# Optimization experiments

Hardware: AMD Instinct MI355X
Metric: run time of the kernel (lower is better)

Reference implementation:

```python
import jax, jax.numpy as jnp
import numpy as np

B, T, C = 4, 2048, 2048
H, G = 16, 4            # num_heads, gqa_factor
HKV = H // G            # kv heads = 4
D = C // H              # head_dim = 128
KV = HKV * D            # kv_embed_dim = 512


def setup_inputs() -> dict:
    key = jax.random.key(0)
    ks = jax.random.split(key, 6)
    w_scale = (2.0 / (C + C)) ** 0.5  # xavier-uniform-ish std
    return {
        "query": jax.random.normal(ks[0], (B, T, C), jnp.float32),
        "key": jax.random.normal(ks[1], (B, T, C), jnp.float32),
        "value": jax.random.normal(ks[2], (B, T, C), jnp.float32),
        "in_proj_weight": jax.random.normal(ks[3], (C + 2 * KV, C), jnp.float32) * w_scale,
        "in_proj_bias": jnp.zeros((C + 2 * KV,), jnp.float32),
        "out_proj_weight": jax.random.normal(ks[4], (C, C), jnp.float32) * w_scale,
        "out_proj_bias": jnp.zeros((C,), jnp.float32),
    }


def reference(query, key, value, in_proj_weight, in_proj_bias, out_proj_weight, out_proj_bias):
    # split fused QKV projection (rows: [C | KV | KV])
    qw, kw, vw = in_proj_weight[:C], in_proj_weight[C:C + KV], in_proj_weight[C + KV:]
    qb, kb, vb = in_proj_bias[:C], in_proj_bias[C:C + KV], in_proj_bias[C + KV:]

    xq = query @ qw.T + qb          # (B,T,C)
    xk = key @ kw.T + kb            # (B,T,KV)
    xv = value @ vw.T + vb          # (B,T,KV)

    # (B,T,G,Hkv,D) -> (B,G,Hkv,T,D)
    xq = xq.reshape(B, T, G, HKV, D).transpose(0, 2, 3, 1, 4)
    # (B,T,Hkv,D) -> (B,Hkv,T,D); broadcast over G in attention
    xk = xk.reshape(B, T, HKV, D).transpose(0, 2, 1, 3)
    xv = xv.reshape(B, T, HKV, D).transpose(0, 2, 1, 3)

    scale = 1.0 / jnp.sqrt(jnp.asarray(D, xq.dtype))
    scores = jnp.einsum("bghtd,bhsd->bghts", xq, xk) * scale  # (B,G,Hkv,T,T)
    causal = jnp.tril(jnp.ones((T, T), bool))
    scores = jnp.where(causal, scores, jnp.finfo(scores.dtype).min)
    attn = jax.nn.softmax(scores, axis=-1)

    xo = jnp.einsum("bghts,bhsd->bghtd", attn, xv)            # (B,G,Hkv,T,D)
    xo = xo.transpose(0, 3, 1, 2, 4).reshape(B, T, C)          # (B,T,C)
    return xo @ out_proj_weight.T + out_proj_bias
```

## Files before the change

### kernel.cpp

```cpp
#include <hip/hip_runtime.h>
#include <hip/hip_bf16.h>
#include <stdint.h>

#define B_ 4
#define T_ 2048
#define C_ 2048
#define H_ 16
#define HKV_ 4
#define D_ 128
#define KV_ 512

typedef __attribute__((ext_vector_type(8))) short bf16x8;
typedef __attribute__((ext_vector_type(4))) float f32x4;

__device__ __forceinline__ unsigned short f2bf(float f) {
    union { float f; unsigned int u; } c;
    c.f = f;
    unsigned int u = c.u;
    u += 0x7FFFu + ((u >> 16) & 1u);
    return (unsigned short)(u >> 16);
}

__global__ __launch_bounds__(256)
void f32_to_bf16(const float* __restrict__ src, unsigned short* __restrict__ dst, int n4)
{
    int i = blockIdx.x * 256 + threadIdx.x;
    if (i < n4) {
        float4 v = ((const float4*)src)[i];
        ushort4 o;
        o.x = f2bf(v.x); o.y = f2bf(v.y); o.z = f2bf(v.z); o.w = f2bf(v.w);
        ((ushort4*)dst)[i] = o;
    }
}

template <typename OutT, bool TRANS>
__global__ __launch_bounds__(256)
void gemm_bt_bias(const __hip_bfloat16* __restrict__ A,
                  const __hip_bfloat16* __restrict__ W,
                  const float* __restrict__ bias,
                  OutT* __restrict__ Cmat,
                  int M, int N, int K)
{
    __shared__ __align__(16) __hip_bfloat16 lA[128 * 32];
    __shared__ __align__(16) __hip_bfloat16 lB[128 * 32];

    const int tid  = threadIdx.x;
    const int wave = tid >> 6;
    const int lane = tid & 63;
    const int m0 = blockIdx.x * 128;
    const int n0 = blockIdx.y * 128;
    const int wm = (wave >> 1) * 64;
    const int wn = (wave & 1) * 64;
    const int srow = lane >> 2;
    const int scol = (lane & 3) * 8;
    const int quad = lane >> 4;
    const int r16  = lane & 15;

    f32x4 acc[4][4];
#pragma unroll
    for (int i = 0; i < 4; ++i)
#pragma unroll
        for (int j = 0; j < 4; ++j)
            acc[i][j] = (f32x4){0.f, 0.f, 0.f, 0.f};

    const __hip_bfloat16* gA = A + (size_t)(m0 + wave * 16 + srow) * K + scol;
    const __hip_bfloat16* gB = W + (size_t)(n0 + wave * 16 + srow) * K + scol;

    for (int k0 = 0; k0 < K; k0 += 32) {
        __builtin_amdgcn_global_load_lds(
            (const __attribute__((address_space(1))) void*)(gA + k0),
            (__attribute__((address_space(3))) void*)(lA + wave * 16 * 32), 16, 0, 0);
        __builtin_amdgcn_global_load_lds(
            (const __attribute__((address_space(1))) void*)(gA + (size_t)64 * K + k0),
            (__attribute__((address_space(3))) void*)(lA + (64 + wave * 16) * 32), 16, 0, 0);
        __builtin_amdgcn_global_load_lds(
            (const __attribute__((address_space(1))) void*)(gB + k0),
            (__attribute__((address_space(3))) void*)(lB + wave * 16 * 32), 16, 0, 0);
        __builtin_amdgcn_global_load_lds(
            (const __attribute__((address_space(1))) void*)(gB + (size_t)64 * K + k0),
            (__attribute__((address_space(3))) void*)(lB + (64 + wave * 16) * 32), 16, 0, 0);
        __syncthreads();

        bf16x8 af[4], bfr[4];
#pragma unroll
        for (int i = 0; i < 4; ++i)
            af[i] = *(const bf16x8*)(lA + (wm + i * 16 + r16) * 32 + quad * 8);
#pragma unroll
        for (int j = 0; j < 4; ++j)
            bfr[j] = *(const bf16x8*)(lB + (wn + j * 16 + r16) * 32 + quad * 8);
#pragma unroll
        for (int i = 0; i < 4; ++i)
#pragma unroll
            for (int j = 0; j < 4; ++j)
                acc[i][j] = __builtin_amdgcn_mfma_f32_16x16x32_bf16(
                    af[i], bfr[j], acc[i][j], 0, 0, 0);
        __syncthreads();
    }

#pragma unroll
    for (int i = 0; i < 4; ++i) {
        const int row = m0 + wm + i * 16 + quad * 4;
#pragma unroll
        for (int j = 0; j < 4; ++j) {
            const int col = n0 + wn + j * 16 + r16;
            const float bb = bias[col];
            if constexpr (TRANS) {
                const int bb_idx = row >> 11;
                const int t = row & (T_ - 1);
                ushort4 o;
                o.x = f2bf(acc[i][j][0] + bb);
                o.y = f2bf(acc[i][j][1] + bb);
                o.z = f2bf(acc[i][j][2] + bb);
                o.w = f2bf(acc[i][j][3] + bb);
                *(ushort4*)((unsigned short*)Cmat +
                            ((size_t)(bb_idx * N + col)) * T_ + t) = o;
            } else {
#pragma unroll
                for (int r = 0; r < 4; ++r) {
                    const float v = acc[i][j][r] + bb;
                    if constexpr (sizeof(OutT) == 4) {
                        Cmat[(size_t)(row + r) * N + col] = v;
                    } else {
                        ((unsigned short*)Cmat)[(size_t)(row + r) * N + col] = f2bf(v);
                    }
                }
            }
        }
    }
}

__global__ __launch_bounds__(512)
void attn_flash(const __hip_bfloat16* __restrict__ xq,
                const __hip_bfloat16* __restrict__ xk,
                const __hip_bfloat16* __restrict__ xvT,
                __hip_bfloat16* __restrict__ xo)
{
    __shared__ __align__(16) __hip_bfloat16 lK[2][64 * 128];
    __shared__ __align__(16) __hip_bfloat16 lV[2][128 * 64];
    __shared__ __align__(16) __hip_bfloat16 lP[8 * 32 * 64];

    const int tid  = threadIdx.x;
    const int wave = tid >> 6;
    const int lane = tid & 63;
    const int quad = lane >> 4;
    const int r16  = lane & 15;
    const int sw8  = (r16 & 7) * 8;
    const int q0 = blockIdx.x * 256;
    const int h  = blockIdx.y;
    const int b  = blockIdx.z;
    const int hkv = h & (HKV_ - 1);
    const int r0 = q0 + wave * 32;
    const float SC2 = 0.12751879215f;
    const float SH2 = 17.3123404907f;

    bf16x8 qf[2][4];
#pragma unroll
    for (int i = 0; i < 2; ++i)
#pragma unroll
        for (int kc = 0; kc < 4; ++kc)
            qf[i][kc] = *(const bf16x8*)(
                xq + ((size_t)(b * T_ + r0 + i * 16 + r16)) * C_ +
                h * D_ + kc * 32 + quad * 8);

    f32x4 oacc[2][8];
#pragma unroll
    for (int i = 0; i < 2; ++i)
#pragma unroll
        for (int db = 0; db < 8; ++db)
            oacc[i][db] = (f32x4){0.f, 0.f, 0.f, 0.f};
    float lrow[2][4];
#pragma unroll
    for (int i = 0; i < 2; ++i)
#pragma unroll
        for (int r = 0; r < 4; ++r) lrow[i][r] = 0.f;

    const __hip_bfloat16* kb = xk + ((size_t)b * T_) * KV_ + hkv * D_;
    const __hip_bfloat16* vb = xvT + ((size_t)(b * KV_ + hkv * D_)) * T_;
    __hip_bfloat16* lPw = lP + wave * 32 * 64;

    const int krl  = lane >> 4;
    const int ksw  = ((lane & 15) ^ (((wave & 1) * 4) + krl)) * 8;
    const int vrl  = lane >> 3;
    const int vsw  = ((lane & 7) ^ vrl) * 8;

    const int ntiles = q0 / 64 + 4;

    auto STAGE = [&](int buf, int tile) {
        const int s0 = tile * 64;
        __hip_bfloat16* lKb = &lK[buf][0];
        __hip_bfloat16* lVb = &lV[buf][0];
#pragma unroll
        for (int q = 0; q < 2; ++q) {
            __builtin_amdgcn_global_load_lds(
                (const __attribute__((address_space(1))) void*)(
                    kb + (size_t)(s0 + q * 32 + wave * 4 + krl) * KV_ + ksw),
                (__attribute__((address_space(3))) void*)(lKb + (q * 32 + wave * 4) * 128),
                16, 0, 0);
            __builtin_amdgcn_global_load_lds(
                (const __attribute__((address_space(1))) void*)(
                    vb + (size_t)(q * 64 + wave * 8 + vrl) * T_ + s0 + vsw),
                (__attribute__((address_space(3))) void*)(lVb + (q * 64 + wave * 8) * 64),
                16, 0, 0);
        }
    };

    STAGE(0, 0);
    __syncthreads();

    for (int tile = 0; tile < ntiles; ++tile) {
        const int cur = tile & 1;
        const int s0 = tile * 64;

        if (tile + 1 < ntiles) STAGE(cur ^ 1, tile + 1);

        const __hip_bfloat16* lKc = &lK[cur][0];
        const __hip_bfloat16* lVc = &lV[cur][0];

        if (s0 <= r0 + 31) {
            const bool diag = (s0 + 63 > r0);

            f32x4 sacc[2][4];
#pragma unroll
            for (int i = 0; i < 2; ++i)
#pragma unroll
                for (int j = 0; j < 4; ++j)
                    sacc[i][j] = (f32x4){0.f, 0.f, 0.f, 0.f};
#pragma unroll
            for (int kc = 0; kc < 4; ++kc) {
                bf16x8 kf[4];
#pragma unroll
                for (int j = 0; j < 4; ++j)
                    kf[j] = *(const bf16x8*)(lKc + (j * 16 + r16) * 128 +
                                             ((kc * 32 + quad * 8) ^ sw8));
#pragma unroll
                for (int i = 0; i < 2; ++i)
#pragma unroll
                    for (int j = 0; j < 4; ++j)
                        sacc[i][j] = __builtin_amdgcn_mfma_f32_16x16x32_bf16(
                            qf[i][kc], kf[j], sacc[i][j], 0, 0, 0);
            }

#pragma unroll
            for (int i = 0; i < 2; ++i) {
#pragma unroll
                for (int j = 0; j < 4; ++j)
#pragma unroll
                    for (int r = 0; r < 4; ++r) {
                        float p = exp2f(fmaf(sacc[i][j][r], SC2, -SH2));
                        if (diag) {
                            const int rr = r0 + i * 16 + quad * 4 + r;
                            const int cc = s0 + j * 16 + r16;
                            if (cc > rr) p = 0.f;
                        }
                        lrow[i][r] += p;
                        const int prow = i * 16 + quad * 4 + r;
                        ((unsigned short*)lPw)[prow * 64 +
                            ((j * 16 + r16) ^ (((quad * 4 + r) & 7) * 8))] = f2bf(p);
                    }
            }

#pragma unroll
            for (int sc = 0; sc < 2; ++sc) {
                bf16x8 pf[2];
#pragma unroll
                for (int i = 0; i < 2; ++i)
                    pf[i] = *(const bf16x8*)(lPw + (i * 16 + r16) * 64 +
                                             ((sc * 32 + quad * 8) ^ sw8));
#pragma unroll
                for (int db = 0; db < 8; ++db) {
                    const bf16x8 vf = *(const bf16x8*)(lVc + (db * 16 + r16) * 64 +
                                                       ((sc * 32 + quad * 8) ^ sw8));
#pragma unroll
                    for (int i = 0; i < 2; ++i)
                        oacc[i][db] = __builtin_amdgcn_mfma_f32_16x16x32_bf16(
                            pf[i], vf, oacc[i][db], 0, 0, 0);
                }
            }
        }
        __syncthreads();
    }

#pragma unroll
    for (int i = 0; i < 2; ++i) {
#pragma unroll
        for (int off = 1; off <= 8; off <<= 1)
#pragma unroll
            for (int r = 0; r < 4; ++r)
                lrow[i][r] += __shfl_xor(lrow[i][r], off);
        float inv[4];
#pragma unroll
        for (int r = 0; r < 4; ++r) inv[r] = 1.0f / lrow[i][r];
#pragma unroll
        for (int db = 0; db < 8; ++db)
#pragma unroll
            for (int r = 0; r < 4; ++r)
                ((unsigned short*)xo)[((size_t)(b * T_ + r0 + i * 16 + quad * 4 + r)) * C_ +
                                      h * D_ + db * 16 + r16] =
                    f2bf(oacc[i][db][r] * inv[r]);
    }
}

extern "C" void kernel_launch(void* const* d_in, const int* in_sizes, int n_in,
                              void* d_out, int out_size, void* d_ws, size_t ws_size,
                              hipStream_t stream)
{
    const float* query = (const float*)d_in[0];
    const float* key   = (const float*)d_in[1];
    const float* value = (const float*)d_in[2];
    const float* ipw   = (const float*)d_in[3];
    const float* ipb   = (const float*)d_in[4];
    const float* opw   = (const float*)d_in[5];
    const float* opb   = (const float*)d_in[6];
    float* out = (float*)d_out;

    const size_t nQ  = (size_t)B_ * T_ * C_;
    const size_t nW  = (size_t)(C_ + 2 * KV_) * C_;
    const size_t nKV = (size_t)B_ * T_ * KV_;

    __hip_bfloat16* qb  = (__hip_bfloat16*)d_ws;
    __hip_bfloat16* wb  = qb + nQ;
    __hip_bfloat16* xq  = wb + nW;
    __hip_bfloat16* xk  = xq + nQ;
    __hip_bfloat16* xvT = xk + nKV;
    __hip_bfloat16* xo  = qb;

    const int M = B_ * T_;
    dim3 blk(256);

    f32_to_bf16<<<(int)(nW / 4 / 256), blk, 0, stream>>>(ipw, (unsigned short*)wb, (int)(nW / 4));
    f32_to_bf16<<<(int)(nQ / 4 / 256), blk, 0, stream>>>(query, (unsigned short*)qb, (int)(nQ / 4));
    gemm_bt_bias<__hip_bfloat16, false><<<dim3(M / 128, C_ / 128), blk, 0, stream>>>(
        qb, wb, ipb, xq, M, C_, C_);

    f32_to_bf16<<<(int)(nQ / 4 / 256), blk, 0, stream>>>(key, (unsigned short*)qb, (int)(nQ / 4));
    gemm_bt_bias<__hip_bfloat16, false><<<dim3(M / 128, KV_ / 128), blk, 0, stream>>>(
        qb, wb + (size_t)C_ * C_, ipb + C_, xk, M, KV_, C_);

    f32_to_bf16<<<(int)(nQ / 4 / 256), blk, 0, stream>>>(value, (unsigned short*)qb, (int)(nQ / 4));
    gemm_bt_bias<__hip_bfloat16, true><<<dim3(M / 128, KV_ / 128), blk, 0, stream>>>(
        qb, wb + (size_t)(C_ + KV_) * C_, ipb + C_ + KV_, xvT, M, KV_, C_);

    attn_flash<<<dim3(T_ / 256, H_, B_), dim3(512), 0, stream>>>(xq, xk, xvT, xo);

    const size_t nOW = (size_t)C_ * C_;
    f32_to_bf16<<<(int)(nOW / 4 / 256), blk, 0, stream>>>(opw, (unsigned short*)wb, (int)(nOW / 4));
    gemm_bt_bias<float, false><<<dim3(M / 128, C_ / 128), blk, 0, stream>>>(
        xo, wb, opb, out, M, C_, C_);
}
```

Before: 751.5 us.

## Load K/V fragments directly from global memory in attention, drop LDS staging

The attention kernel no longer stages K and V tiles into double-buffered shared memory with async global-to-LDS loads and block-wide barriers. Each wave now reads its K and V MFMA fragments straight from global memory, relying on L1/L2 caching, and runs its own causal tile count with no block synchronization. Blocks shrink to 256 threads covering 128 query rows, which cuts LDS use to the P scratch only and doubles the grid. The change removes barrier stalls and causal-imbalance idling. In exchange it adds redundant global traffic across waves and exposes more load latency with no prefetch.

```diff
diff --git a/kernel.cpp b/kernel.cpp
--- a/kernel.cpp
+++ b/kernel.cpp
@@ -129,15 +129,13 @@
     }
 }
 
-__global__ __launch_bounds__(512)
+__global__ __launch_bounds__(256)
 void attn_flash(const __hip_bfloat16* __restrict__ xq,
                 const __hip_bfloat16* __restrict__ xk,
                 const __hip_bfloat16* __restrict__ xvT,
                 __hip_bfloat16* __restrict__ xo)
 {
-    __shared__ __align__(16) __hip_bfloat16 lK[2][64 * 128];
-    __shared__ __align__(16) __hip_bfloat16 lV[2][128 * 64];
-    __shared__ __align__(16) __hip_bfloat16 lP[8 * 32 * 64];
+    __shared__ __align__(16) __hip_bfloat16 lP[4][32 * 64];
 
     const int tid  = threadIdx.x;
     const int wave = tid >> 6;
@@ -145,7 +143,7 @@
     const int quad = lane >> 4;
     const int r16  = lane & 15;
     const int sw8  = (r16 & 7) * 8;
-    const int q0 = blockIdx.x * 256;
+    const int q0 = blockIdx.x * 128;
     const int h  = blockIdx.y;
     const int b  = blockIdx.z;
     const int hkv = h & (HKV_ - 1);
@@ -176,108 +174,76 @@
 
     const __hip_bfloat16* kb = xk + ((size_t)b * T_) * KV_ + hkv * D_;
     const __hip_bfloat16* vb = xvT + ((size_t)(b * KV_ + hkv * D_)) * T_;
-    __hip_bfloat16* lPw = lP + wave * 32 * 64;
-
-    const int krl  = lane >> 4;
-    const int ksw  = ((lane & 15) ^ (((wave & 1) * 4) + krl)) * 8;
-    const int vrl  = lane >> 3;
-    const int vsw  = ((lane & 7) ^ vrl) * 8;
-
-    const int ntiles = q0 / 64 + 4;
-
-    auto STAGE = [&](int buf, int tile) {
+    __hip_bfloat16* lPw = &lP[wave][0];
+
+    const int ntiles = r0 / 64 + 1;
+    for (int tile = 0; tile < ntiles; ++tile) {
         const int s0 = tile * 64;
-        __hip_bfloat16* lKb = &lK[buf][0];
-        __hip_bfloat16* lVb = &lV[buf][0];
-#pragma unroll
-        for (int q = 0; q < 2; ++q) {
-            __builtin_amdgcn_global_load_lds(
-                (const __attribute__((address_space(1))) void*)(
-                    kb + (size_t)(s0 + q * 32 + wave * 4 + krl) * KV_ + ksw),
-                (__attribute__((address_space(3))) void*)(lKb + (q * 32 + wave * 4) * 128),
-                16, 0, 0);
-            __builtin_amdgcn_global_load_lds(
-                (const __attribute__((address_space(1))) void*)(
-                    vb + (size_t)(q * 64 + wave * 8 + vrl) * T_ + s0 + vsw),
-                (__attribute__((address_space(3))) void*)(lVb + (q * 64 + wave * 8) * 64),
-                16, 0, 0);
+        const bool diag = (s0 + 63 > r0);
+
+        f32x4 sacc[2][4];
+#pragma unroll
+        for (int i = 0; i < 2; ++i)
+#pragma unroll
+            for (int j = 0; j < 4; ++j)
+                sacc[i][j] = (f32x4){0.f, 0.f, 0.f, 0.f};
+#pragma unroll
+        for (int kc = 0; kc < 4; ++kc) {
+            bf16x8 kf[4];
+#pragma unroll
+            for (int j = 0; j < 4; ++j)
+                kf[j] = *(const bf16x8*)(
+                    kb + (size_t)(s0 + j * 16 + r16) * KV_ + kc * 32 + quad * 8);
+#pragma unroll
+            for (int i = 0; i < 2; ++i)
+#pragma unroll
+                for (int j = 0; j < 4; ++j)
+                    sacc[i][j] = __builtin_amdgcn_mfma_f32_16x16x32_bf16(
+                        qf[i][kc], kf[j], sacc[i][j], 0, 0, 0);
         }
-    };
-
-    STAGE(0, 0);
-    __syncthreads();
-
-    for (int tile = 0; tile < ntiles; ++tile) {
-        const int cur = tile & 1;
-        const int s0 = tile * 64;
-
-        if (tile + 1 < ntiles) STAGE(cur ^ 1, tile + 1);
-
-        const __hip_bfloat16* lKc = &lK[cur][0];
-        const __hip_bfloat16* lVc = &lV[cur][0];
-
-        if (s0 <= r0 + 31) {
-            const bool diag = (s0 + 63 > r0);
-
-            f32x4 sacc[2][4];
+
+#pragma unroll
+        for (int i = 0; i < 2; ++i) {
+#pragma unroll
+            for (int j = 0; j < 4; ++j)
+#pragma unroll
+                for (int r = 0; r < 4; ++r) {
+                    float p = exp2f(fmaf(sacc[i][j][r], SC2, -SH2));
+                    if (diag) {
+                        const int rr = r0 + i * 16 + quad * 4 + r;
+                        const int cc = s0 + j * 16 + r16;
+                        if (cc > rr) p = 0.f;
+                    }
+                    lrow[i][r] += p;
+                    const int prow = i * 16 + quad * 4 + r;
+                    ((unsigned short*)lPw)[prow * 64 +
+                        ((j * 16 + r16) ^ (((quad * 4 + r) & 7) * 8))] = f2bf(p);
+                }
+        }
+
+#pragma unroll
+        for (int sc = 0; sc < 2; ++sc) {
+            bf16x8 pf[2];
 #pragma unroll
             for (int i = 0; i < 2; ++i)
-#pragma unroll
-                for (int j = 0; j < 4; ++j)
-                    sacc[i][j] = (f32x4){0.f, 0.f, 0.f, 0.f};
-#pragma unroll
-            for (int kc = 0; kc < 4; ++kc) {
-                bf16x8 kf[4];
-#pragma unroll
-                for (int j = 0; j < 4; ++j)
-                    kf[j] = *(const bf16x8*)(lKc + (j * 16 + r16) * 128 +
-                                             ((kc * 32 + quad * 8) ^ sw8));
-#pragma unroll
-                for (int i = 0; i < 2; ++i)
-#pragma unroll
-                    for (int j = 0; j < 4; ++j)
-                        sacc[i][j] = __builtin_amdgcn_mfma_f32_16x16x32_bf16(
-                            qf[i][kc], kf[j], sacc[i][j], 0, 0, 0);
-            }
-
-#pragma unroll
-            for (int i = 0; i < 2; ++i) {
-#pragma unroll
-                for (int j = 0; j < 4; ++j)
-#pragma unroll
-                    for (int r = 0; r < 4; ++r) {
-                        float p = exp2f(fmaf(sacc[i][j][r], SC2, -SH2));
-                        if (diag) {
-                            const int rr = r0 + i * 16 + quad * 4 + r;
-                            const int cc = s0 + j * 16 + r16;
-                            if (cc > rr) p = 0.f;
-                        }
-                        lrow[i][r] += p;
-                        const int prow = i * 16 + quad * 4 + r;
-                        ((unsigned short*)lPw)[prow * 64 +
-                            ((j * 16 + r16) ^ (((quad * 4 + r) & 7) * 8))] = f2bf(p);
-                    }
-            }
-
-#pragma unroll
-            for (int sc = 0; sc < 2; ++sc) {
-                bf16x8 pf[2];
-#pragma unroll
-                for (int i = 0; i < 2; ++i)
-                    pf[i] = *(const bf16x8*)(lPw + (i * 16 + r16) * 64 +
-                                             ((sc * 32 + quad * 8) ^ sw8));
-#pragma unroll
-                for (int db = 0; db < 8; ++db) {
-                    const bf16x8 vf = *(const bf16x8*)(lVc + (db * 16 + r16) * 64 +
-                                                       ((sc * 32 + quad * 8) ^ sw8));
+                pf[i] = *(const bf16x8*)(lPw + (i * 16 + r16) * 64 +
+                                         ((sc * 32 + quad * 8) ^ sw8));
+#pragma unroll
+            for (int dbb = 0; dbb < 2; ++dbb) {
+                bf16x8 vf4[4];
+#pragma unroll
+                for (int t = 0; t < 4; ++t)
+                    vf4[t] = *(const bf16x8*)(
+                        vb + (size_t)((dbb * 4 + t) * 16 + r16) * T_ +
+                        s0 + sc * 32 + quad * 8);
+#pragma unroll
+                for (int t = 0; t < 4; ++t)
 #pragma unroll
                     for (int i = 0; i < 2; ++i)
-                        oacc[i][db] = __builtin_amdgcn_mfma_f32_16x16x32_bf16(
-                            pf[i], vf, oacc[i][db], 0, 0, 0);
-                }
+                        oacc[i][dbb * 4 + t] = __builtin_amdgcn_mfma_f32_16x16x32_bf16(
+                            pf[i], vf4[t], oacc[i][dbb * 4 + t], 0, 0, 0);
             }
         }
-        __syncthreads();
     }
 
 #pragma unroll
@@ -340,7 +306,7 @@
     gemm_bt_bias<__hip_bfloat16, true><<<dim3(M / 128, KV_ / 128), blk, 0, stream>>>(
         qb, wb + (size_t)(C_ + KV_) * C_, ipb + C_ + KV_, xvT, M, KV_, C_);
 
-    attn_flash<<<dim3(T_ / 256, H_, B_), dim3(512), 0, stream>>>(xq, xk, xvT, xo);
+    attn_flash<<<dim3(T_ / 128, H_, B_), blk, 0, stream>>>(xq, xk, xvT, xo);
 
     const size_t nOW = (size_t)C_ * C_;
     f32_to_bf16<<<(int)(nOW / 4 / 256), blk, 0, stream>>>(opw, (unsigned short*)wb, (int)(nOW / 4));
```

Result: slower. 994.9 us (+32.4%).
